# Kernel tuning notes

Measured on AMD Instinct MI355X. Metric: run time of the kernel, lower is better.

## Reference

```python
import jax, jax.numpy as jnp
import numpy as np

B = 16          # batch (number of point clouds)
N = 16384       # total points across batch
H = 512         # hidden_size
E = 64          # traj_embed_size
T = 8           # max_traj_len
EB = 72         # euler_bins = 360 // 5
OUT = EB * 3 + 2  # action_mlp output: 216 rot logits + open + stop = 218
TEMP = 1.0


def setup_inputs() -> dict:
    key = jax.random.key(0)
    ks = jax.random.split(key, 8)
    rng = np.random.default_rng(0)
    # ragged segment sizes, each >= 256, summing exactly to N
    counts = rng.multinomial(N - B * 256, np.ones(B) / B) + 256
    s = 0.02
    return {
        "point_embeds": jax.random.normal(ks[0], (N, H), jnp.float32),
        "coords": jax.random.normal(ks[1], (N, 3), jnp.float32),
        "traj_emb": jax.random.normal(ks[2], (T, E), jnp.float32) * s,
        "hm_w1": jax.random.normal(ks[3], (H + E, H), jnp.float32) * s,
        "hm_b1": jnp.zeros((H,), jnp.float32),
        "hm_w2": jax.random.normal(ks[4], (H, 4), jnp.float32) * s,
        "hm_b2": jnp.zeros((4,), jnp.float32),
        "act_w1": jax.random.normal(ks[5], (H + E, H), jnp.float32) * s,
        "act_b1": jnp.zeros((H,), jnp.float32),
        "act_w2": jax.random.normal(ks[6], (H, OUT), jnp.float32) * s,
        "act_b2": jnp.zeros((OUT,), jnp.float32),
        "npoints_in_batch": jnp.asarray(counts, jnp.int32),
    }


def _lrelu(x):
    return jnp.where(x >= 0, x, 0.02 * x)


def reference(point_embeds, coords, traj_emb, hm_w1, hm_b1, hm_w2, hm_b2,
              act_w1, act_b1, act_w2, act_b2, npoints_in_batch):
    n = point_embeds.shape[0]
    # segment id per point (replaces torch.split over ragged batch)
    seg = jnp.repeat(jnp.arange(B), npoints_in_batch, total_repeat_length=n)  # (N,)

    # expand with trajectory-step embedding: (N, T, H+E)
    pe = jnp.concatenate([
        jnp.broadcast_to(point_embeds[:, None, :], (n, T, H)),
        jnp.broadcast_to(traj_emb[None, :, :], (n, T, E)),
    ], axis=-1)

    # heatmap MLP: (N, T, 4) = [heatmap logit, delta xyz]
    hm = _lrelu(pe @ hm_w1 + hm_b1) @ hm_w2 + hm_b2
    logits = hm[..., 0]                                # (N, T)

    # per-segment stable softmax over points
    m = jax.ops.segment_max(logits, seg, num_segments=B)          # (B, T)
    e = jnp.exp((logits - m[seg]) / TEMP)                         # (N, T)
    z = jax.ops.segment_sum(e, seg, num_segments=B)               # (B, T)
    h = e / z[seg]                                                # (N, T)

    new_coords = coords[:, None, :] + hm[..., 1:]                 # (N, T, 3)
    xt = jax.ops.segment_sum(h[..., None] * new_coords, seg, num_segments=B)  # (B, T, 3)

    # reduce == 'max': per-segment max pooling of point embeds
    pc = jax.ops.segment_max(pe, seg, num_segments=B)             # (B, T, H+E)
    ae = _lrelu(pc @ act_w1 + act_b1) @ act_w2 + act_b2           # (B, T, 218)

    xr = ae[..., :EB * 3].reshape(B, T, EB, 3)  # euler_disc logits
    xo = ae[..., -2]
    xstop = ae[..., -1]
    return (xt, xr, xo, xstop)
```

## Files before the change

kernel.cpp:

```cpp
#include <hip/hip_runtime.h>
#include <math.h>

typedef unsigned short u16;
typedef unsigned int u32;

#define NPTS 16384
#define HID  512
#define TT   8
#define TE   64
#define NB   16
#define OUTC 218

typedef short s16x8 __attribute__((ext_vector_type(8)));
typedef float f32x4 __attribute__((ext_vector_type(4)));

__device__ __forceinline__ float bf2f(u16 u) {
  return __uint_as_float(((u32)u) << 16);
}
__device__ __forceinline__ u16 f2bf(float f) {
  u32 x = __float_as_uint(f);
  x += 0x7fffu + ((x >> 16) & 1u);
  return (u16)(x >> 16);
}
__device__ __forceinline__ float lrelu(float h) { return fmaxf(h, 0.02f * h); }

__device__ __forceinline__ float rd(const void* p, size_t i, bool f32) {
  return f32 ? ((const float*)p)[i] : bf2f(((const u16*)p)[i]);
}
__device__ __forceinline__ void wr(void* p, size_t i, bool f32, float v) {
  if (f32) ((float*)p)[i] = v;
  else ((u16*)p)[i] = f2bf(v);
}

__global__ __launch_bounds__(256) void prep_conv_kernel(
    const void* __restrict__ hm_w1, const void* __restrict__ hm_b1,
    const void* __restrict__ traj, const void* __restrict__ hm_w2,
    const void* __restrict__ hm_b2, const void* __restrict__ aw1,
    const void* __restrict__ ab1, const void* __restrict__ pe,
    const int* __restrict__ npts, float* __restrict__ vprime,
    float* __restrict__ w2f, float* __restrict__ b2f,
    float* __restrict__ avp, u16* __restrict__ Bth,
    float* __restrict__ partial, int* __restrict__ flag) {
  const int tid = threadIdx.x, blk = blockIdx.x;
  __shared__ int sflag;
  if (tid == 0) sflag = 0;
  __syncthreads();
  {
    const u16* p16 = (const u16*)pe;
    int c = 0;
    for (int i = tid; i < 8192; i += 256)
      if ((p16[i] & 0x7F80u) == 0x7F80u) c = 1;
    if (c) sflag = 1;
  }
  __syncthreads();
  const bool f32 = sflag != 0;
  if (blk < 8) {
    const int t = blk;
    for (int j = tid; j < 512; j += 256) {
      float acc = rd(hm_b1, j, f32);
      for (int e = 0; e < 64; ++e)
        acc = fmaf(rd(traj, t * 64 + e, f32),
                   rd(hm_w1, (size_t)(512 + e) * 512 + j, f32), acc);
      vprime[t * 512 + j] = acc;
    }
  } else if (blk < 16) {
    const int t = blk - 8;
    for (int j = tid; j < 512; j += 256) {
      float acc = rd(ab1, j, f32);
      for (int e = 0; e < 64; ++e)
        acc = fmaf(rd(traj, t * 64 + e, f32),
                   rd(aw1, (size_t)(512 + e) * 512 + j, f32), acc);
      avp[t * 512 + j] = acc;
    }
  } else if (blk == 16) {
    if (tid == 0) flag[0] = f32 ? 1 : 0;
    for (int i = tid; i < 2048; i += 256) w2f[i] = rd(hm_w2, i, f32);
    if (tid < 4) b2f[tid] = rd(hm_b2, tid, f32);
  } else if (blk < 145) {
    const int g = (blk - 17) * 256 + tid;
    const int j = g & 511;
    const int kbase = (g >> 9) * 8;
    const int seg = (j >> 4) * 16 + (kbase >> 5);
    const int lane_ = (((kbase >> 3) & 3) << 4) | (j & 15);
    const size_t dst = ((size_t)seg * 64 + lane_) * 8;
    s16x8 hv;
    if (f32) {
      const float* W1 = (const float*)hm_w1;
#pragma unroll
      for (int i = 0; i < 8; ++i)
        hv[i] = (short)f2bf(W1[(size_t)(kbase + i) * 512 + j]);
      *(s16x8*)&Bth[dst] = hv;
    } else {
      const u16* W1 = (const u16*)hm_w1;
#pragma unroll
      for (int i = 0; i < 8; ++i) hv[i] = (short)W1[(size_t)(kbase + i) * 512 + j];
      *(s16x8*)&Bth[dst] = hv;
    }
  } else {
    const int blk2 = blk - 145;
    const int b = blk2 >> 4, c = blk2 & 15;
    int s0 = 0, cnt = 0;
    for (int i = 0; i < 16; ++i) {
      const int v = npts[i];
      if (i < b) s0 += v;
      if (i == b) cnt = v;
    }
    const int chunk = (cnt + 15) >> 4;
    const int r0 = s0 + c * chunk;
    int r1 = r0 + chunk;
    const int rend = s0 + cnt;
    if (r1 > rend) r1 = rend;
    const int j2 = tid;
    float m0 = -1e30f, m1 = -1e30f;
    if (f32) {
      const float* pf = (const float*)pe;
      for (int n = r0; n < r1; ++n) {
        const float2 v = *(const float2*)(pf + (size_t)n * 512 + 2 * j2);
        m0 = fmaxf(m0, v.x);
        m1 = fmaxf(m1, v.y);
      }
    } else {
      const u32* p32 = (const u32*)pe;
      for (int n = r0; n < r1; ++n) {
        const u32 v = p32[(size_t)n * 256 + j2];
        m0 = fmaxf(m0, bf2f((u16)(v & 0xffffu)));
        m1 = fmaxf(m1, bf2f((u16)(v >> 16)));
      }
    }
    partial[(size_t)blk2 * 512 + 2 * j2] = m0;
    partial[(size_t)blk2 * 512 + 2 * j2 + 1] = m1;
  }
}

#define SU_STRIDE 516
__global__ __launch_bounds__(1024, 4) void gemm_fused(
    const void* __restrict__ A, const u16* __restrict__ Bth,
    const float* __restrict__ vprime, const float* __restrict__ w2f,
    const float* __restrict__ b2f, const void* __restrict__ coords,
    float* __restrict__ logits, float* __restrict__ nc,
    const int* __restrict__ flag) {
  const bool f32 = flag[0] != 0;
  __shared__ __attribute__((aligned(16))) char smem[64 * SU_STRIDE * 4];
  __shared__ float4 sred[512];
  __shared__ float sW2[2048];
  u16* sAh = (u16*)smem;
  const int tid = threadIdx.x;
  const int rb = blockIdx.x * 64;
  for (int i = tid; i < 2048; i += 1024) sW2[i] = w2f[i];
#pragma unroll
  for (int it = 0; it < 4; ++it) {
    const int c = tid + it * 1024;
    const int row = ((c >> 10) << 4) | (c & 15);
    const int kc = (((c >> 6) & 15) << 2) | ((c >> 4) & 3);
    if (f32) {
      const float* src = (const float*)A + (size_t)(rb + row) * 512 + kc * 8;
      const float4 x0 = *(const float4*)(src);
      const float4 x1 = *(const float4*)(src + 4);
      const float xs[8] = {x0.x, x0.y, x0.z, x0.w, x1.x, x1.y, x1.z, x1.w};
      s16x8 hv;
#pragma unroll
      for (int i = 0; i < 8; ++i) hv[i] = (short)f2bf(xs[i]);
      *(s16x8*)&sAh[c * 8] = hv;
    } else {
      *(s16x8*)&sAh[c * 8] =
          *(const s16x8*)((const u16*)A + (size_t)(rb + row) * 512 + kc * 8);
    }
  }
  __syncthreads();
  const int wave = tid >> 6, lane = tid & 63;
  f32x4 acc[4][2];
#pragma unroll
  for (int rt = 0; rt < 4; ++rt)
#pragma unroll
    for (int ct = 0; ct < 2; ++ct) acc[rt][ct] = (f32x4){0.f, 0.f, 0.f, 0.f};
  const int bbase = (wave * 2 * 16 * 64 + lane) * 8;
#define LDB(H, ks)                                                             \
  {                                                                            \
    H[0] = *(const s16x8*)&Bth[bbase + (ks) * 512];                            \
    H[1] = *(const s16x8*)&Bth[bbase + 8192 + (ks) * 512];                     \
  }
#define LDA(ks)                                                                \
  {                                                                            \
    _Pragma("unroll") for (int rt = 0; rt < 4; ++rt) {                         \
      const int aoff = ((rt * 16 + (ks)) * 64 + lane) * 8;                     \
      ah[rt] = *(const s16x8*)&sAh[aoff];                                      \
    }                                                                          \
  }
#define MM(H)                                                                  \
  _Pragma("unroll") for (int rt = 0; rt < 4; ++rt)                             \
      _Pragma("unroll") for (int ct = 0; ct < 2; ++ct) {                       \
    acc[rt][ct] = __builtin_amdgcn_mfma_f32_16x16x32_bf16(ah[rt], H[ct],       \
                                                          acc[rt][ct], 0, 0,   \
                                                          0);                  \
  }
  {
    s16x8 ah[4];
    s16x8 bh0[2], bh1[2], bh2[2], bh3[2];
    LDB(bh0, 0);
    LDB(bh1, 1);
    LDB(bh2, 2);
#pragma unroll
    for (int ks = 0; ks < 16; ks += 4) {
      LDB(bh3, ks + 3);
      LDA(ks);
      MM(bh0);
      if (ks + 4 < 16) LDB(bh0, ks + 4);
      LDA(ks + 1);
      MM(bh1);
      if (ks + 5 < 16) LDB(bh1, ks + 5);
      LDA(ks + 2);
      MM(bh2);
      if (ks + 6 < 16) LDB(bh2, ks + 6);
      LDA(ks + 3);
      MM(bh3);
    }
  }
#undef LDB
#undef LDA
#undef MM
  __syncthreads();
  float* sU = (float*)smem;
  const int lr = lane & 15, orow = (lane >> 4) * 4;
#pragma unroll
  for (int rt = 0; rt < 4; ++rt)
#pragma unroll
    for (int ct = 0; ct < 2; ++ct) {
      const int col = (wave * 2 + ct) * 16 + lr;
#pragma unroll
      for (int r = 0; r < 4; ++r)
        sU[(rt * 16 + orow + r) * SU_STRIDE + col] = acc[rt][ct][r];
    }
  __syncthreads();
  const int p = tid & 511, half = tid >> 9;
  const int ln = p >> 3, t = p & 7;
  const int n = rb + ln;
  const float* su = sU + ln * SU_STRIDE + half * 256;
  const float* vp = vprime + t * 512 + half * 256;
  const float4* w4 = (const float4*)sW2 + half * 64 * 4;
  float a0 = 0.f, a1 = 0.f, a2 = 0.f, a3 = 0.f;
#pragma unroll 4
  for (int j4 = 0; j4 < 64; ++j4) {
    const float4 uu = *(const float4*)(su + j4 * 4);
    const float4 vv = *(const float4*)(vp + j4 * 4);
    const float4 w_0 = w4[j4 * 4 + 0];
    const float4 w_1 = w4[j4 * 4 + 1];
    const float4 w_2 = w4[j4 * 4 + 2];
    const float4 w_3 = w4[j4 * 4 + 3];
    float h;
    h = lrelu(uu.x + vv.x);
    a0 = fmaf(h, w_0.x, a0); a1 = fmaf(h, w_0.y, a1);
    a2 = fmaf(h, w_0.z, a2); a3 = fmaf(h, w_0.w, a3);
    h = lrelu(uu.y + vv.y);
    a0 = fmaf(h, w_1.x, a0); a1 = fmaf(h, w_1.y, a1);
    a2 = fmaf(h, w_1.z, a2); a3 = fmaf(h, w_1.w, a3);
    h = lrelu(uu.z + vv.z);
    a0 = fmaf(h, w_2.x, a0); a1 = fmaf(h, w_2.y, a1);
    a2 = fmaf(h, w_2.z, a2); a3 = fmaf(h, w_2.w, a3);
    h = lrelu(uu.w + vv.w);
    a0 = fmaf(h, w_3.x, a0); a1 = fmaf(h, w_3.y, a1);
    a2 = fmaf(h, w_3.z, a2); a3 = fmaf(h, w_3.w, a3);
  }
  if (half) sred[p] = make_float4(a0, a1, a2, a3);
  __syncthreads();
  if (!half) {
    const float4 r = sred[p];
    a0 += r.x; a1 += r.y; a2 += r.z; a3 += r.w;
    logits[(size_t)n * 8 + t] = a0 + b2f[0];
    float* o = nc + ((size_t)n * 8 + t) * 3;
    o[0] = rd(coords, (size_t)n * 3 + 0, f32) + a1 + b2f[1];
    o[1] = rd(coords, (size_t)n * 3 + 1, f32) + a2 + b2f[2];
    o[2] = rd(coords, (size_t)n * 3 + 2, f32) + a3 + b2f[3];
  }
}

__global__ __launch_bounds__(256) void softact_kernel(
    const float* __restrict__ logits, const float* __restrict__ nc,
    const int* __restrict__ npts, const float* __restrict__ partial,
    const void* __restrict__ aw1, const float* __restrict__ avp,
    float* __restrict__ hid, void* __restrict__ out,
    const int* __restrict__ flag) {
  const bool f32 = flag[0] != 0;
  const int tid = threadIdx.x;
  if (blockIdx.x < 128) {
    const int b = blockIdx.x >> 3, t = blockIdx.x & 7;
    int s0 = 0, cnt = 0;
    for (int i = 0; i < 16; ++i) {
      const int v = npts[i];
      if (i < b) s0 += v;
      if (i == b) cnt = v;
    }
    __shared__ float wm[4];
    __shared__ float red[4][4];
    float m = -1e30f;
    for (int i = tid; i < cnt; i += 256)
      m = fmaxf(m, logits[(size_t)(s0 + i) * 8 + t]);
#pragma unroll
    for (int o = 32; o > 0; o >>= 1) m = fmaxf(m, __shfl_down(m, o, 64));
    if ((tid & 63) == 0) wm[tid >> 6] = m;
    __syncthreads();
    const float mt = fmaxf(fmaxf(wm[0], wm[1]), fmaxf(wm[2], wm[3]));
    float z = 0.f, x = 0.f, y = 0.f, w = 0.f;
    for (int i = tid; i < cnt; i += 256) {
      const size_t g = (size_t)(s0 + i) * 8 + t;
      const float e = expf(logits[g] - mt);
      const float* c3 = nc + g * 3;
      z += e;
      x = fmaf(e, c3[0], x);
      y = fmaf(e, c3[1], y);
      w = fmaf(e, c3[2], w);
    }
#pragma unroll
    for (int o = 32; o > 0; o >>= 1) {
      z += __shfl_down(z, o, 64);
      x += __shfl_down(x, o, 64);
      y += __shfl_down(y, o, 64);
      w += __shfl_down(w, o, 64);
    }
    if ((tid & 63) == 0) {
      red[0][tid >> 6] = z; red[1][tid >> 6] = x;
      red[2][tid >> 6] = y; red[3][tid >> 6] = w;
    }
    __syncthreads();
    if (tid == 0) {
      const float Z = red[0][0] + red[0][1] + red[0][2] + red[0][3];
      const float X = red[1][0] + red[1][1] + red[1][2] + red[1][3];
      const float Y = red[2][0] + red[2][1] + red[2][2] + red[2][3];
      const float W = red[3][0] + red[3][1] + red[3][2] + red[3][3];
      wr(out, (size_t)(b * 8 + t) * 3 + 0, f32, X / Z);
      wr(out, (size_t)(b * 8 + t) * 3 + 1, f32, Y / Z);
      wr(out, (size_t)(b * 8 + t) * 3 + 2, f32, W / Z);
    }
  } else {
    const int blk2 = blockIdx.x - 128;
    const int b = blk2 >> 3, jt = blk2 & 7;
    __shared__ float spc[512];
    __shared__ float sred2[4][64];
    for (int k = tid; k < 512; k += 256) {
      float m = -1e30f;
#pragma unroll
      for (int c = 0; c < 16; ++c)
        m = fmaxf(m, partial[(size_t)(b * 16 + c) * 512 + k]);
      spc[k] = m;
    }
    __syncthreads();
    const int jj = tid & 63, kq = tid >> 6;
    const int j = jt * 64 + jj;
    const int kb = kq * 128;
    float a0 = 0.f, a1 = 0.f, a2 = 0.f, a3 = 0.f;
    if (f32) {
      const float* W = (const float*)aw1 + (size_t)kb * 512 + j;
#pragma unroll 4
      for (int k = 0; k < 128; k += 4) {
        a0 = fmaf(spc[kb + k + 0], W[(size_t)(k + 0) * 512], a0);
        a1 = fmaf(spc[kb + k + 1], W[(size_t)(k + 1) * 512], a1);
        a2 = fmaf(spc[kb + k + 2], W[(size_t)(k + 2) * 512], a2);
        a3 = fmaf(spc[kb + k + 3], W[(size_t)(k + 3) * 512], a3);
      }
    } else {
      const u16* W = (const u16*)aw1 + (size_t)kb * 512 + j;
#pragma unroll 4
      for (int k = 0; k < 128; k += 4) {
        a0 = fmaf(spc[kb + k + 0], bf2f(W[(size_t)(k + 0) * 512]), a0);
        a1 = fmaf(spc[kb + k + 1], bf2f(W[(size_t)(k + 1) * 512]), a1);
        a2 = fmaf(spc[kb + k + 2], bf2f(W[(size_t)(k + 2) * 512]), a2);
        a3 = fmaf(spc[kb + k + 3], bf2f(W[(size_t)(k + 3) * 512]), a3);
      }
    }
    sred2[kq][jj] = (a0 + a1) + (a2 + a3);
    __syncthreads();
    if (kq == 0) {
      const float s = (sred2[0][jj] + sred2[1][jj]) + (sred2[2][jj] + sred2[3][jj]);
#pragma unroll
      for (int t = 0; t < 8; ++t)
        hid[(size_t)(b * 8 + t) * 512 + j] = lrelu(s + avp[t * 512 + j]);
    }
  }
}

__global__ __launch_bounds__(256) void act_out_kernel(
    const float* __restrict__ hid, const void* __restrict__ aw2,
    const void* __restrict__ ab2, void* __restrict__ out,
    const int* __restrict__ flag) {
  const bool f32 = flag[0] != 0;
  __shared__ float sh[512];
  const int row = blockIdx.x, tid = threadIdx.x;
  for (int i = tid; i < 512; i += 256) sh[i] = hid[(size_t)row * 512 + i];
  __syncthreads();
  if (tid < OUTC) {
    float a0 = 0.f, a1 = 0.f, a2 = 0.f, a3 = 0.f;
    if (f32) {
      const float* W = (const float*)aw2 + tid;
#pragma unroll 8
      for (int j = 0; j < 512; j += 4) {
        a0 = fmaf(sh[j + 0], W[(size_t)(j + 0) * OUTC], a0);
        a1 = fmaf(sh[j + 1], W[(size_t)(j + 1) * OUTC], a1);
        a2 = fmaf(sh[j + 2], W[(size_t)(j + 2) * OUTC], a2);
        a3 = fmaf(sh[j + 3], W[(size_t)(j + 3) * OUTC], a3);
      }
    } else {
      const u16* W = (const u16*)aw2 + tid;
#pragma unroll 8
      for (int j = 0; j < 512; j += 4) {
        a0 = fmaf(sh[j + 0], bf2f(W[(size_t)(j + 0) * OUTC]), a0);
        a1 = fmaf(sh[j + 1], bf2f(W[(size_t)(j + 1) * OUTC]), a1);
        a2 = fmaf(sh[j + 2], bf2f(W[(size_t)(j + 2) * OUTC]), a2);
        a3 = fmaf(sh[j + 3], bf2f(W[(size_t)(j + 3) * OUTC]), a3);
      }
    }
    const float o = rd(ab2, tid, f32) + ((a0 + a1) + (a2 + a3));
    if (tid < 216)
      wr(out, 384 + (size_t)row * 216 + tid, f32, o);
    else if (tid == 216)
      wr(out, 384 + 27648 + row, f32, o);
    else
      wr(out, 384 + 27648 + 128 + row, f32, o);
  }
}

extern "C" void kernel_launch(void* const* d_in, const int* in_sizes, int n_in,
                              void* d_out, int out_size, void* d_ws,
                              size_t ws_size, hipStream_t stream) {
  (void)in_sizes; (void)n_in; (void)out_size; (void)ws_size;
  const void* pe     = d_in[0];
  const void* coords = d_in[1];
  const void* traj   = d_in[2];
  const void* hm_w1  = d_in[3];
  const void* hm_b1  = d_in[4];
  const void* hm_w2  = d_in[5];
  const void* hm_b2  = d_in[6];
  const void* aw1    = d_in[7];
  const void* ab1    = d_in[8];
  const void* aw2    = d_in[9];
  const void* ab2    = d_in[10];
  const int* npts    = (const int*)d_in[11];

  char* ws = (char*)d_ws;
  int*   flag    = (int*)(ws + 0);
  float* avp     = (float*)(ws + 256);
  float* hid     = (float*)(ws + 16896);
  u16*   Bth     = (u16*)(ws + 524288);
  float* vprime  = (float*)(ws + 34078720);
  float* w2f     = (float*)(ws + 34095104);
  float* b2f     = (float*)(ws + 34103296);
  float* logits  = (float*)(ws + 34103552);
  float* nc      = (float*)(ws + 34627840);
  float* partial = (float*)(ws + 36200704);

  prep_conv_kernel<<<401, 256, 0, stream>>>(hm_w1, hm_b1, traj, hm_w2, hm_b2,
                                            aw1, ab1, pe, npts, vprime, w2f,
                                            b2f, avp, Bth, partial, flag);
  gemm_fused<<<NPTS / 64, 1024, 0, stream>>>(pe, Bth, vprime, w2f, b2f,
                                             coords, logits, nc, flag);
  softact_kernel<<<256, 256, 0, stream>>>(logits, nc, npts, partial, aw1, avp,
                                          hid, d_out, flag);
  act_out_kernel<<<128, 256, 0, stream>>>(hid, aw2, ab2, d_out, flag);
}
```

Baseline: 171.4 us.

## Halve gemm_fused row tile to 32 and split epilogue four ways

The fused heatmap GEMM kernel now handles 32 rows per block instead of 64, doubling the grid to 512 blocks and shrinking the shared-memory footprint. The B-operand prefetch pipeline drops from 4 stages to 2. The second-layer epilogue is split across four thread groups of 128 hidden units, combined through a 3-slot shared reduction. The hm_w2 weights are now read straight from global memory instead of being staged in shared memory. The aim is more blocks and occupancy per CU, at the cost of reloading the full B matrix for every 32 rows and a shallower prefetch.

Result: slower. 204.7 us (+19.4%).

```diff
diff --git a/kernel.cpp b/kernel.cpp
--- a/kernel.cpp
+++ b/kernel.cpp
@@ -140,15 +140,13 @@
     float* __restrict__ logits, float* __restrict__ nc,
     const int* __restrict__ flag) {
   const bool f32 = flag[0] != 0;
-  __shared__ __attribute__((aligned(16))) char smem[64 * SU_STRIDE * 4];
-  __shared__ float4 sred[512];
-  __shared__ float sW2[2048];
+  __shared__ __attribute__((aligned(16))) char smem[32 * SU_STRIDE * 4];
+  __shared__ float4 sred[3][256];
   u16* sAh = (u16*)smem;
   const int tid = threadIdx.x;
-  const int rb = blockIdx.x * 64;
-  for (int i = tid; i < 2048; i += 1024) sW2[i] = w2f[i];
-#pragma unroll
-  for (int it = 0; it < 4; ++it) {
+  const int rb = blockIdx.x * 32;
+#pragma unroll
+  for (int it = 0; it < 2; ++it) {
     const int c = tid + it * 1024;
     const int row = ((c >> 10) << 4) | (c & 15);
     const int kc = (((c >> 6) & 15) << 2) | ((c >> 4) & 3);
@@ -168,9 +166,9 @@
   }
   __syncthreads();
   const int wave = tid >> 6, lane = tid & 63;
-  f32x4 acc[4][2];
-#pragma unroll
-  for (int rt = 0; rt < 4; ++rt)
+  f32x4 acc[2][2];
+#pragma unroll
+  for (int rt = 0; rt < 2; ++rt)
 #pragma unroll
     for (int ct = 0; ct < 2; ++ct) acc[rt][ct] = (f32x4){0.f, 0.f, 0.f, 0.f};
   const int bbase = (wave * 2 * 16 * 64 + lane) * 8;
@@ -181,38 +179,30 @@
   }
 #define LDA(ks)                                                                \
   {                                                                            \
-    _Pragma("unroll") for (int rt = 0; rt < 4; ++rt) {                         \
+    _Pragma("unroll") for (int rt = 0; rt < 2; ++rt) {                         \
       const int aoff = ((rt * 16 + (ks)) * 64 + lane) * 8;                     \
       ah[rt] = *(const s16x8*)&sAh[aoff];                                      \
     }                                                                          \
   }
 #define MM(H)                                                                  \
-  _Pragma("unroll") for (int rt = 0; rt < 4; ++rt)                             \
+  _Pragma("unroll") for (int rt = 0; rt < 2; ++rt)                             \
       _Pragma("unroll") for (int ct = 0; ct < 2; ++ct) {                       \
     acc[rt][ct] = __builtin_amdgcn_mfma_f32_16x16x32_bf16(ah[rt], H[ct],       \
                                                           acc[rt][ct], 0, 0,   \
                                                           0);                  \
   }
   {
-    s16x8 ah[4];
-    s16x8 bh0[2], bh1[2], bh2[2], bh3[2];
+    s16x8 ah[2];
+    s16x8 bh0[2], bh1[2];
     LDB(bh0, 0);
-    LDB(bh1, 1);
-    LDB(bh2, 2);
-#pragma unroll
-    for (int ks = 0; ks < 16; ks += 4) {
-      LDB(bh3, ks + 3);
+#pragma unroll
+    for (int ks = 0; ks < 16; ks += 2) {
+      LDB(bh1, ks + 1);
       LDA(ks);
       MM(bh0);
-      if (ks + 4 < 16) LDB(bh0, ks + 4);
+      if (ks + 2 < 16) LDB(bh0, ks + 2);
       LDA(ks + 1);
       MM(bh1);
-      if (ks + 5 < 16) LDB(bh1, ks + 5);
-      LDA(ks + 2);
-      MM(bh2);
-      if (ks + 6 < 16) LDB(bh2, ks + 6);
-      LDA(ks + 3);
-      MM(bh3);
     }
   }
 #undef LDB
@@ -222,7 +212,7 @@
   float* sU = (float*)smem;
   const int lr = lane & 15, orow = (lane >> 4) * 4;
 #pragma unroll
-  for (int rt = 0; rt < 4; ++rt)
+  for (int rt = 0; rt < 2; ++rt)
 #pragma unroll
     for (int ct = 0; ct < 2; ++ct) {
       const int col = (wave * 2 + ct) * 16 + lr;
@@ -231,15 +221,15 @@
         sU[(rt * 16 + orow + r) * SU_STRIDE + col] = acc[rt][ct][r];
     }
   __syncthreads();
-  const int p = tid & 511, half = tid >> 9;
+  const int p = tid & 255, q = tid >> 8;
   const int ln = p >> 3, t = p & 7;
   const int n = rb + ln;
-  const float* su = sU + ln * SU_STRIDE + half * 256;
-  const float* vp = vprime + t * 512 + half * 256;
-  const float4* w4 = (const float4*)sW2 + half * 64 * 4;
+  const float* su = sU + ln * SU_STRIDE + q * 128;
+  const float* vp = vprime + t * 512 + q * 128;
+  const float4* w4 = (const float4*)w2f + q * 128;
   float a0 = 0.f, a1 = 0.f, a2 = 0.f, a3 = 0.f;
 #pragma unroll 4
-  for (int j4 = 0; j4 < 64; ++j4) {
+  for (int j4 = 0; j4 < 32; ++j4) {
     const float4 uu = *(const float4*)(su + j4 * 4);
     const float4 vv = *(const float4*)(vp + j4 * 4);
     const float4 w_0 = w4[j4 * 4 + 0];
@@ -260,11 +250,14 @@
     a0 = fmaf(h, w_3.x, a0); a1 = fmaf(h, w_3.y, a1);
     a2 = fmaf(h, w_3.z, a2); a3 = fmaf(h, w_3.w, a3);
   }
-  if (half) sred[p] = make_float4(a0, a1, a2, a3);
-  __syncthreads();
-  if (!half) {
-    const float4 r = sred[p];
-    a0 += r.x; a1 += r.y; a2 += r.z; a3 += r.w;
+  if (q) sred[q - 1][p] = make_float4(a0, a1, a2, a3);
+  __syncthreads();
+  if (!q) {
+#pragma unroll
+    for (int s = 0; s < 3; ++s) {
+      const float4 r = sred[s][p];
+      a0 += r.x; a1 += r.y; a2 += r.z; a3 += r.w;
+    }
     logits[(size_t)n * 8 + t] = a0 + b2f[0];
     float* o = nc + ((size_t)n * 8 + t) * 3;
     o[0] = rd(coords, (size_t)n * 3 + 0, f32) + a1 + b2f[1];
@@ -449,7 +442,7 @@
   prep_conv_kernel<<<401, 256, 0, stream>>>(hm_w1, hm_b1, traj, hm_w2, hm_b2,
                                             aw1, ab1, pe, npts, vprime, w2f,
                                             b2f, avp, Bth, partial, flag);
-  gemm_fused<<<NPTS / 64, 1024, 0, stream>>>(pe, Bth, vprime, w2f, b2f,
+  gemm_fused<<<NPTS / 32, 1024, 0, stream>>>(pe, Bth, vprime, w2f, b2f,
                                              coords, logits, nc, flag);
   softact_kernel<<<256, 256, 0, stream>>>(logits, nc, npts, partial, aw1, avp,
                                           hid, d_out, flag);
```
